# Kernel optimization log

Measured on AMD Instinct MI355X. Metric: run time of the kernel, lower is better.

The kernel has to match this reference:

```python
import jax, jax.numpy as jnp
import numpy as np

B, L, D, H, E, K = 8, 2048, 512, 512, 256, 30


def setup_inputs() -> dict:
    key = jax.random.key(0)
    ks = jax.random.split(key, 10)
    init = lambda k, shape: (jax.random.normal(k, shape, jnp.float32) * 0.02)
    x = jax.random.normal(ks[0], (B, L, D), jnp.float32)
    # lengths in [L//2, L]; first one forced to L so max(x_lengths) == L (matches torch mask shape)
    rest = jax.random.randint(ks[9], (B - 1,), L // 2, L + 1).astype(jnp.int32)
    x_lengths = jnp.concatenate([jnp.array([L], jnp.int32), rest])
    return {
        "x": x,
        "w_g_w": init(ks[1], (D, H)), "w_g_b": init(ks[2], (H,)),
        "t1_w": init(ks[3], (D, E)), "t1_b": init(ks[4], (E,)),
        "t2_w": init(ks[5], (D, E)), "t2_b": init(ks[6], (E,)),
        "w_z_w": init(ks[7], (H, D)), "w_z_b": init(ks[8], (D,)),
        "x_lengths": x_lengths,
    }


def reference(x, w_g_w, w_g_b, t1_w, t1_b, t2_w, t2_b, w_z_w, w_z_b, x_lengths):
    # x: [B, L, D]
    x_prime = x @ w_g_w + w_g_b                      # [B, L, H]
    x1 = x @ t1_w + t1_b                             # [B, L, E]
    x2 = x @ t2_w + t2_b                             # [B, L, E]
    inter = jnp.einsum("bie,bje->bij", x1, x2)      # [B, L, L]
    att = jax.nn.softmax(inter, axis=-1)             # embedded_gaussian
    # key-side length mask (masks.permute([0,2,1]) in torch -> [B,1,L])
    mask = (jnp.arange(L)[None, :] < x_lengths[:, None]).astype(att.dtype)
    att = att * mask[:, None, :]
    att = att / jnp.sum(att, axis=-1, keepdims=True)
    # top-k clipping + scatter back into a zero matrix, then renormalize
    topk, idx = jax.lax.top_k(att, K)                # [B, L, K]
    bi = jnp.arange(B)[:, None, None]
    ri = jnp.arange(L)[None, :, None]
    att = jnp.zeros_like(att).at[bi, ri, idx].set(topk)
    att = att / jnp.sum(att, axis=-1, keepdims=True)
    y = att @ x_prime                                # [B, L, H]
    y = y @ w_z_w + w_z_b                            # [B, L, D]
    return x + y
```

## Files before the change

kernel.cpp:

```cpp
#include <hip/hip_runtime.h>


typedef _Float16 h2   __attribute__((ext_vector_type(2)));
typedef _Float16 h4   __attribute__((ext_vector_type(4)));
typedef _Float16 h8   __attribute__((ext_vector_type(8)));
typedef float    f32x4 __attribute__((ext_vector_type(4)));

__device__ __forceinline__ h2 as_h2(float f) {
    union { float f; h2 h; } u; u.f = f; return u.h;
}
__device__ __forceinline__ float packh2(float a, float b) {
    union { h2 h; float f; } u; u.h.x = (_Float16)a; u.h.y = (_Float16)b; return u.f;
}

__global__ __launch_bounds__(256) void k0_tp(
    const float* __restrict__ src, _Float16* __restrict__ dst, int Kd, int Nd)
{
    __shared__ float tile[32][33];
    const int t = threadIdx.x;
    const int n0 = blockIdx.x * 32, k0 = blockIdx.y * 32;
    const int r = t >> 3, c = (t & 7) * 4;
    *(float4*)&tile[r][c] = *(const float4*)(src + (size_t)(k0 + r) * Nd + n0 + c);
    __syncthreads();
    h4 hv;
    hv.x = (_Float16)tile[c + 0][r];
    hv.y = (_Float16)tile[c + 1][r];
    hv.z = (_Float16)tile[c + 2][r];
    hv.w = (_Float16)tile[c + 3][r];
    *(h4*)(dst + (size_t)(n0 + r) * Kd + k0 + c) = hv;
}

__global__ __launch_bounds__(256) void k1_mfma(
    const float* __restrict__ x, const _Float16* __restrict__ wT,
    const float* __restrict__ bg, const float* __restrict__ b1,
    const float* __restrict__ b2,
    float* __restrict__ xph, float* __restrict__ x1p, float4* __restrict__ x2tn4)
{
    __shared__ __align__(16) char lds_raw[40960];
    _Float16* Alds = (_Float16*)lds_raw;
    _Float16* Blds = (_Float16*)(lds_raw + 8192);

    const int t = threadIdx.x;
    const int m0 = blockIdx.x * 64;
    const int cb = blockIdx.y;
    const int n0 = cb * 256;
    const int lane = t & 63, w = t >> 6;
    const int arow = lane & 15, ak = (lane >> 4) * 8;

    f32x4 acc[4][4];
    #pragma unroll
    for (int i = 0; i < 4; ++i)
        #pragma unroll
        for (int j = 0; j < 4; ++j) acc[i][j] = (f32x4){0.f, 0.f, 0.f, 0.f};

    for (int k0 = 0; k0 < 512; k0 += 64) {
        __syncthreads();
        {
            const int r = t >> 2, c0 = (t & 3) * 16;
            const float* src = x + (size_t)(m0 + r) * 512 + k0 + c0;
            #pragma unroll
            for (int hvi = 0; hvi < 2; ++hvi) {
                float4 u0 = *(const float4*)(src + hvi * 8);
                float4 u1 = *(const float4*)(src + hvi * 8 + 4);
                h8 hv;
                hv[0] = (_Float16)u0.x; hv[1] = (_Float16)u0.y;
                hv[2] = (_Float16)u0.z; hv[3] = (_Float16)u0.w;
                hv[4] = (_Float16)u1.x; hv[5] = (_Float16)u1.y;
                hv[6] = (_Float16)u1.z; hv[7] = (_Float16)u1.w;
                *(h8*)(Alds + r * 64 + c0 + hvi * 8) = hv;
            }
        }
        {
            #pragma unroll
            for (int i = 0; i < 8; ++i) {
                int idx = t + i * 256;
                int row = idx >> 3, ch = idx & 7;
                *(float4*)(Blds + row * 64 + ch * 8) =
                    *(const float4*)(wT + (size_t)(n0 + row) * 512 + k0 + ch * 8);
            }
        }
        __syncthreads();

        #pragma unroll
        for (int kk = 0; kk < 2; ++kk) {
            h8 af[4], bf[4];
            #pragma unroll
            for (int rb = 0; rb < 4; ++rb)
                af[rb] = *(const h8*)(Alds + (rb * 16 + arow) * 64 + kk * 32 + ak);
            #pragma unroll
            for (int cf = 0; cf < 4; ++cf)
                bf[cf] = *(const h8*)(Blds + (w * 64 + cf * 16 + arow) * 64 + kk * 32 + ak);
            #pragma unroll
            for (int rb = 0; rb < 4; ++rb)
                #pragma unroll
                for (int cf = 0; cf < 4; ++cf)
                    acc[rb][cf] = __builtin_amdgcn_mfma_f32_16x16x32_f16(
                        af[rb], bf[cf], acc[rb][cf], 0, 0, 0);
        }
    }

    const float* bias = (cb < 2) ? (bg + cb * 256) : (cb == 2 ? b1 : b2);

    if (cb < 3) {
        float* dst; int epbase; size_t rstr;
        if (cb < 2) { dst = xph; epbase = cb * 128; rstr = 256; }
        else        { dst = x1p; epbase = 0;        rstr = 128; }
        #pragma unroll
        for (int cf = 0; cf < 4; ++cf) {
            const int c = w * 64 + cf * 16 + arow;
            const float bv = bias[c];
            #pragma unroll
            for (int rb = 0; rb < 4; ++rb) {
                #pragma unroll
                for (int j = 0; j < 4; ++j) {
                    float v = acc[rb][cf][j] + bv;
                    float o = __shfl_xor(v, 1);
                    if ((lane & 1) == 0) {
                        int row = m0 + rb * 16 + (lane >> 4) * 4 + j;
                        dst[(size_t)row * rstr + epbase + (c >> 1)] = packh2(v, o);
                    }
                }
            }
        }
    } else {
        __syncthreads();
        float* T = (float*)lds_raw;
        #pragma unroll
        for (int cf = 0; cf < 4; ++cf) {
            const int c = w * 64 + cf * 16 + arow;
            const float bv = bias[c];
            #pragma unroll
            for (int rb = 0; rb < 4; ++rb) {
                #pragma unroll
                for (int j = 0; j < 4; ++j) {
                    float v = acc[rb][cf][j] + bv;
                    float o = __shfl_xor(v, 1);
                    if ((lane & 1) == 0)
                        T[(c >> 1) * 68 + rb * 16 + (lane >> 4) * 4 + j] = packh2(v, o);
                }
            }
        }
        __syncthreads();
        const int bb = m0 >> 11, j0 = m0 & 2047;
        #pragma unroll
        for (int g = 0; g < 8; ++g) {
            int slot = t + g * 256;
            int jt = slot >> 9;
            int ks = (slot >> 6) & 7;
            int l  = slot & 63;
            int eg = l >> 4, jc = l & 15;
            const float* Tp = T + (ks * 16 + eg * 4) * 68 + jt * 16 + jc;
            float4 v;
            v.x = Tp[0]; v.y = Tp[68]; v.z = Tp[136]; v.w = Tp[204];
            x2tn4[(((size_t)bb * 128 + (j0 >> 4) + jt) * 8 + ks) * 64 + l] = v;
        }
    }
}

__global__ __launch_bounds__(512, 4) void k2_attn(
    const float* __restrict__ x1p, const float4* __restrict__ x2tn4,
    const float* __restrict__ xph, const int* __restrict__ xlen,
    float* __restrict__ yah)
{
    __shared__ unsigned scU[16][1024];
    __shared__ unsigned cand[16][64];
    __shared__ unsigned tkp[16][30];
    __shared__ float    wvs[16][30];
    __shared__ int      tki[16][30];
    __shared__ float    vin[16];
    __shared__ unsigned rowmax[16];
    __shared__ int      cntA[16][2];
    __shared__ int      cntF[16];

    const int t  = threadIdx.x;
    const int b  = blockIdx.x & 7;
    const int i0 = (blockIdx.x >> 3) * 16;
    const int len = xlen[b];
    const int lane = t & 63, wid = t >> 6;

    ((unsigned*)cand)[t] = 0u;
    ((unsigned*)cand)[t + 512] = 0u;
    if (t < 32) cntA[t >> 1][t & 1] = 0;
    if (t < 16) cntF[t] = 0;

    h8 afr[8];
    {
        const int ar = lane & 15;
        const float* x1row = x1p + ((size_t)b * 2048 + i0 + ar) * 128 + (lane >> 4) * 4;
        #pragma unroll
        for (int ks = 0; ks < 8; ++ks)
            afr[ks] = *(const h8*)(x1row + ks * 16);
    }

    const float4* x2b = x2tn4 + ((size_t)b * 128) * 8 * 64 + lane;
    const int jcol  = lane & 15;
    const int rbase = (lane >> 4) * 4;

#define LOADT(H, NT, DST)                                                   \
    {                                                                       \
        const float4* pb_ = x2b + (size_t)(((H) * 64 + wid * 8 + (NT)) * 8) * 64; \
        _Pragma("unroll")                                                   \
        for (int ks = 0; ks < 8; ++ks)                                      \
            DST[ks] = *(const h8*)(pb_ + ks * 64);                          \
    }

#define MFMAT(H, NT, SRC)                                                   \
    {                                                                       \
        const int j_ = (H) * 1024 + wid * 128 + (NT) * 16 + jcol;           \
        const int cs_ = wid * 128 + (NT) * 16 + jcol;                       \
        f32x4 acc = (f32x4){0.f, 0.f, 0.f, 0.f};                            \
        _Pragma("unroll")                                                   \
        for (int ks = 0; ks < 8; ++ks)                                      \
            acc = __builtin_amdgcn_mfma_f32_16x16x32_f16(afr[ks], SRC[ks], acc, 0, 0, 0); \
        const unsigned tag = (unsigned)(2047 - j_);                         \
        const bool valid = (j_ < len);                                      \
        _Pragma("unroll")                                                   \
        for (int jj = 0; jj < 4; ++jj) {                                    \
            unsigned bb = __float_as_uint(acc[jj]);                         \
            bb = bb ^ (0x80000000u | (unsigned)((int)bb >> 31));            \
            scU[rbase + jj][cs_] = valid ? ((bb & 0xFFFFF800u) | tag) : 0u; \
        }                                                                   \
    }

    #pragma unroll
    for (int h = 0; h < 2; ++h) {
        {
            h8 va[8], vb[8];
            LOADT(h, 0, va)
            LOADT(h, 1, vb)
            MFMAT(h, 0, va)  LOADT(h, 2, va)
            MFMAT(h, 1, vb)  LOADT(h, 3, vb)
            MFMAT(h, 2, va)  LOADT(h, 4, va)
            MFMAT(h, 3, vb)  LOADT(h, 5, vb)
            MFMAT(h, 4, va)  LOADT(h, 6, va)
            MFMAT(h, 5, vb)  LOADT(h, 7, vb)
            MFMAT(h, 6, va)
            MFMAT(h, 7, vb)
        }
        __syncthreads();

        #pragma unroll
        for (int rr = 0; rr < 2; ++rr) {
            const int row = wid * 2 + rr;
            unsigned u0[16];
            #pragma unroll
            for (int c = 0; c < 4; ++c)
                *(uint4*)&u0[c * 4] = *(const uint4*)&scU[row][lane * 4 + c * 256];

            unsigned P = 0u;
            for (int bit = 31; bit >= 0; --bit) {
                const unsigned cd = P | (1u << bit);
                int cnt = 0;
                #pragma unroll
                for (int q = 0; q < 16; ++q)
                    cnt += (int)__popcll(__ballot(u0[q] >= cd));
                if (cnt >= 30) P = cd;
            }
            #pragma unroll
            for (int q = 0; q < 16; ++q) {
                if (u0[q] >= P && u0[q] != 0u) {
                    int s = atomicAdd(&cntA[row][h], 1);
                    cand[row][h * 30 + s] = u0[q];
                }
            }
        }
        __syncthreads();
    }
#undef LOADT
#undef MFMAT

    #pragma unroll
    for (int rr = 0; rr < 2; ++rr) {
        const int row = wid * 2 + rr;
        unsigned v = (lane < 60) ? cand[row][lane] : 0u;
        unsigned lm = v;
        #pragma unroll
        for (int off = 32; off > 0; off >>= 1) {
            unsigned o = (unsigned)__shfl_xor((int)lm, off);
            lm = lm > o ? lm : o;
        }
        if (lane == 0) rowmax[row] = lm;

        unsigned P = 0u;
        for (int bit = 31; bit >= 0; --bit) {
            const unsigned cd = P | (1u << bit);
            int cnt = (int)__popcll(__ballot(v >= cd));
            if (cnt >= 30) P = cd;
        }
        if (v >= P && v != 0u) {
            int s = atomicAdd(&cntF[row], 1);
            tkp[row][s] = v;
        }
    }
    __syncthreads();

    {
        const int r = t >> 5, k = t & 31;
        if (k < 30) {
            unsigned u = tkp[r][k];
            unsigned m0 = rowmax[r] & 0xFFFFF800u;
            unsigned ub = u & 0xFFFFF800u;
            unsigned bb0 = (m0 & 0x80000000u) ? (m0 ^ 0x80000000u) : ~m0;
            unsigned bbk = (ub & 0x80000000u) ? (ub ^ 0x80000000u) : ~ub;
            float s0 = __uint_as_float(bb0);
            float sk = __uint_as_float(bbk);
            wvs[r][k] = __expf(sk - s0);
            tki[r][k] = 2047 - (int)(u & 0x7FFu);
        }
    }
    __syncthreads();
    if (t < 16) {
        float s = 0.f;
        #pragma unroll
        for (int k = 0; k < 30; ++k) s += wvs[t][k];
        vin[t] = 1.f / s;
    }
    __syncthreads();

    const int g  = t >> 8;
    const int hp = t & 255;
    for (int r = g * 8; r < g * 8 + 8; ++r) {
        float y0 = 0.f, y1 = 0.f;
        #pragma unroll
        for (int k = 0; k < 30; ++k) {
            int j = tki[r][k];
            float wv = wvs[r][k];
            h2 u = as_h2(xph[((size_t)b * 2048 + j) * 256 + hp]);
            y0 = fmaf(wv, (float)u.x, y0);
            y1 = fmaf(wv, (float)u.y, y1);
        }
        const float inv = vin[r];
        yah[((size_t)b * 2048 + i0 + r) * 256 + hp] = packh2(y0 * inv, y1 * inv);
    }
}

__global__ __launch_bounds__(256) void k3_mfma(
    const float* __restrict__ yah, const _Float16* __restrict__ wzT,
    const float* __restrict__ bz, const float* __restrict__ x,
    float* __restrict__ out)
{
    __shared__ __align__(16) char lds_raw[40960];
    _Float16* Alds = (_Float16*)lds_raw;
    _Float16* Blds = (_Float16*)(lds_raw + 8192);

    const int t = threadIdx.x;
    const int m0 = blockIdx.x * 64;
    const int n0 = blockIdx.y * 256;
    const int lane = t & 63, w = t >> 6;
    const int arow = lane & 15, ak = (lane >> 4) * 8;

    f32x4 acc[4][4];
    #pragma unroll
    for (int i = 0; i < 4; ++i)
        #pragma unroll
        for (int j = 0; j < 4; ++j) acc[i][j] = (f32x4){0.f, 0.f, 0.f, 0.f};

    for (int k0 = 0; k0 < 512; k0 += 64) {
        __syncthreads();
        {
            const int r = t >> 2, c0 = (t & 3) * 8;
            const float4* src = (const float4*)(yah + (size_t)(m0 + r) * 256 + k0 / 2 + c0);
            float4* dst = (float4*)(Alds + r * 64 + c0 * 2);
            dst[0] = src[0]; dst[1] = src[1];
        }
        {
            #pragma unroll
            for (int i = 0; i < 8; ++i) {
                int idx = t + i * 256;
                int row = idx >> 3, ch = idx & 7;
                *(float4*)(Blds + row * 64 + ch * 8) =
                    *(const float4*)(wzT + (size_t)(n0 + row) * 512 + k0 + ch * 8);
            }
        }
        __syncthreads();

        #pragma unroll
        for (int kk = 0; kk < 2; ++kk) {
            h8 af[4], bf[4];
            #pragma unroll
            for (int rb = 0; rb < 4; ++rb)
                af[rb] = *(const h8*)(Alds + (rb * 16 + arow) * 64 + kk * 32 + ak);
            #pragma unroll
            for (int cf = 0; cf < 4; ++cf)
                bf[cf] = *(const h8*)(Blds + (w * 64 + cf * 16 + arow) * 64 + kk * 32 + ak);
            #pragma unroll
            for (int rb = 0; rb < 4; ++rb)
                #pragma unroll
                for (int cf = 0; cf < 4; ++cf)
                    acc[rb][cf] = __builtin_amdgcn_mfma_f32_16x16x32_f16(
                        af[rb], bf[cf], acc[rb][cf], 0, 0, 0);
        }
    }

    #pragma unroll
    for (int cf = 0; cf < 4; ++cf) {
        const int c = n0 + w * 64 + cf * 16 + arow;
        const float bv = bz[c];
        #pragma unroll
        for (int rb = 0; rb < 4; ++rb) {
            #pragma unroll
            for (int j = 0; j < 4; ++j) {
                int row = m0 + rb * 16 + (lane >> 4) * 4 + j;
                out[(size_t)row * 512 + c] =
                    acc[rb][cf][j] + bv + x[(size_t)row * 512 + c];
            }
        }
    }
}

extern "C" void kernel_launch(void* const* d_in, const int* in_sizes, int n_in,
                              void* d_out, int out_size, void* d_ws, size_t ws_size,
                              hipStream_t stream)
{
    (void)in_sizes; (void)n_in; (void)out_size; (void)ws_size;

    const float* x   = (const float*)d_in[0];
    const float* wg  = (const float*)d_in[1];
    const float* bg  = (const float*)d_in[2];
    const float* w1  = (const float*)d_in[3];
    const float* b1  = (const float*)d_in[4];
    const float* w2  = (const float*)d_in[5];
    const float* b2  = (const float*)d_in[6];
    const float* wzw = (const float*)d_in[7];
    const float* wzb = (const float*)d_in[8];
    const int* xlen  = (const int*)d_in[9];
    float* outp      = (float*)d_out;

    char* ws = (char*)d_ws;
    _Float16* wT   = (_Float16*)(ws);
    _Float16* wzT  = (_Float16*)(ws + 1u * 1024 * 1024);
    float* x1pw    = (float*)(ws +  2u * 1024 * 1024);
    float4* x2tnw  = (float4*)(ws + 10u * 1024 * 1024);
    float* xphw    = (float*)(ws + 18u * 1024 * 1024);
    float* yahw    = (float*)(ws + 34u * 1024 * 1024);

    hipLaunchKernelGGL(k0_tp, dim3(16, 16), dim3(256), 0, stream, wg,  wT,            512, 512);
    hipLaunchKernelGGL(k0_tp, dim3(8, 16),  dim3(256), 0, stream, w1,  wT + 512*512,  512, 256);
    hipLaunchKernelGGL(k0_tp, dim3(8, 16),  dim3(256), 0, stream, w2,  wT + 768*512,  512, 256);
    hipLaunchKernelGGL(k0_tp, dim3(16, 16), dim3(256), 0, stream, wzw, wzT,           512, 512);

    hipLaunchKernelGGL(k1_mfma, dim3(256, 4), dim3(256), 0, stream,
                       x, wT, bg, b1, b2, xphw, x1pw, x2tnw);
    hipLaunchKernelGGL(k2_attn, dim3(1024), dim3(512), 0, stream,
                       x1pw, x2tnw, xphw, xlen, yahw);
    hipLaunchKernelGGL(k3_mfma, dim3(256, 2), dim3(256), 0, stream,
                       yahw, wzT, wzb, x, outp);
}
```

Measured before the change: 235.0 us.

## Process two rows per wave in top-k radix select and prefetch next half

Result: slower. 283.7 us (+20.7%).

```diff
diff --git a/kernel.cpp b/kernel.cpp
--- a/kernel.cpp
+++ b/kernel.cpp
@@ -222,52 +222,70 @@
         }                                                                   \
     }
 
-    #pragma unroll
-    for (int h = 0; h < 2; ++h) {
-        {
-            h8 va[8], vb[8];
-            LOADT(h, 0, va)
-            LOADT(h, 1, vb)
-            MFMAT(h, 0, va)  LOADT(h, 2, va)
-            MFMAT(h, 1, vb)  LOADT(h, 3, vb)
-            MFMAT(h, 2, va)  LOADT(h, 4, va)
-            MFMAT(h, 3, vb)  LOADT(h, 5, vb)
-            MFMAT(h, 4, va)  LOADT(h, 6, va)
-            MFMAT(h, 5, vb)  LOADT(h, 7, vb)
-            MFMAT(h, 6, va)
-            MFMAT(h, 7, vb)
-        }
-        __syncthreads();
-
-        #pragma unroll
-        for (int rr = 0; rr < 2; ++rr) {
-            const int row = wid * 2 + rr;
-            unsigned u0[16];
-            #pragma unroll
-            for (int c = 0; c < 4; ++c)
-                *(uint4*)&u0[c * 4] = *(const uint4*)&scU[row][lane * 4 + c * 256];
-
-            unsigned P = 0u;
-            for (int bit = 31; bit >= 0; --bit) {
-                const unsigned cd = P | (1u << bit);
-                int cnt = 0;
-                #pragma unroll
-                for (int q = 0; q < 16; ++q)
-                    cnt += (int)__popcll(__ballot(u0[q] >= cd));
-                if (cnt >= 30) P = cd;
-            }
-            #pragma unroll
-            for (int q = 0; q < 16; ++q) {
-                if (u0[q] >= P && u0[q] != 0u) {
-                    int s = atomicAdd(&cntA[row][h], 1);
-                    cand[row][h * 30 + s] = u0[q];
-                }
-            }
-        }
-        __syncthreads();
-    }
+#define TOPK_HALF(H)                                                        \
+    {                                                                       \
+        const int row_ = wid * 2 + (lane >> 5);                             \
+        const int sl_  = lane & 31;                                         \
+        unsigned u0[32];                                                    \
+        _Pragma("unroll")                                                   \
+        for (int c = 0; c < 32; ++c) u0[c] = scU[row_][sl_ + c * 32];       \
+        const bool hi_ = (lane >= 32);                                      \
+        unsigned P = 0u;                                                    \
+        for (int bit = 31; bit >= 0; --bit) {                               \
+            const unsigned cd = P | (1u << bit);                            \
+            int cA = 0, cB = 0;                                             \
+            _Pragma("unroll")                                               \
+            for (int q = 0; q < 32; ++q) {                                  \
+                unsigned long long m_ = __ballot(u0[q] >= cd);              \
+                cA += (int)__popcll(m_ & 0xFFFFFFFFull);                    \
+                cB += (int)__popcll(m_ >> 32);                              \
+            }                                                               \
+            const int cnt = hi_ ? cB : cA;                                  \
+            if (cnt >= 30) P = cd;                                          \
+        }                                                                   \
+        _Pragma("unroll")                                                   \
+        for (int q = 0; q < 32; ++q) {                                      \
+            if (u0[q] >= P && u0[q] != 0u) {                                \
+                int s = atomicAdd(&cntA[row_][H], 1);                       \
+                cand[row_][(H) * 30 + s] = u0[q];                           \
+            }                                                               \
+        }                                                                   \
+    }
+
+    h8 va[8], vb[8];
+    LOADT(0, 0, va)
+    LOADT(0, 1, vb)
+    MFMAT(0, 0, va)  LOADT(0, 2, va)
+    MFMAT(0, 1, vb)  LOADT(0, 3, vb)
+    MFMAT(0, 2, va)  LOADT(0, 4, va)
+    MFMAT(0, 3, vb)  LOADT(0, 5, vb)
+    MFMAT(0, 4, va)  LOADT(0, 6, va)
+    MFMAT(0, 5, vb)  LOADT(0, 7, vb)
+    MFMAT(0, 6, va)
+    MFMAT(0, 7, vb)
+    __syncthreads();
+
+    LOADT(1, 0, va)
+
+    TOPK_HALF(0)
+    __syncthreads();
+
+    LOADT(1, 1, vb)
+    MFMAT(1, 0, va)  LOADT(1, 2, va)
+    MFMAT(1, 1, vb)  LOADT(1, 3, vb)
+    MFMAT(1, 2, va)  LOADT(1, 4, va)
+    MFMAT(1, 3, vb)  LOADT(1, 5, vb)
+    MFMAT(1, 4, va)  LOADT(1, 6, va)
+    MFMAT(1, 5, vb)  LOADT(1, 7, vb)
+    MFMAT(1, 6, va)
+    MFMAT(1, 7, vb)
+    __syncthreads();
+
+    TOPK_HALF(1)
+    __syncthreads();
 #undef LOADT
 #undef MFMAT
+#undef TOPK_HALF
 
     #pragma unroll
     for (int rr = 0; rr < 2; ++rr) {
```
